# Kernel tuning notes

Hardware: AMD Instinct MI355X
Metric: run time of the kernel (lower is better)

The kernel has to match this reference:

```python
import jax, jax.numpy as jnp
import numpy as np

D, NH, NKV, HD, DFF, W, PLD = 2048, 8, 2, 256, 8192, 512, 256
EPS = 1e-6

def rmsnorm(x, w):
    # Gemma-style RMSNorm with (1 + weight) scaling
    return x * jax.lax.rsqrt(jnp.mean(x * x, axis=-1, keepdims=True) + EPS) * (1.0 + w)

def rmsnorm_nw(x):
    # v_norm: weightless RMSNorm
    return x * jax.lax.rsqrt(jnp.mean(x * x, axis=-1, keepdims=True) + EPS)

def rotate_half(x):
    x1, x2 = jnp.split(x, 2, axis=-1)
    return jnp.concatenate([-x2, x1], axis=-1)

def setup_inputs() -> dict:
    key = jax.random.key(0)
    ks = jax.random.split(key, 24)
    w = lambda k, shp, s=0.02: (jax.random.normal(k, shp, dtype=jnp.float32) * s)
    inp = {
        "hidden_states": jax.random.normal(ks[0], (1, 1, D), dtype=jnp.float32),
        "cos": jax.random.uniform(ks[1], (1, 1, HD), dtype=jnp.float32),
        "sin": jax.random.uniform(ks[2], (1, 1, HD), dtype=jnp.float32),
        "mask": jnp.zeros((1, 1, 1, W), dtype=jnp.float32),
        "kv_cache": jnp.zeros((2, NKV, W, HD), dtype=jnp.float32),
        "per_layer": jax.random.normal(ks[3], (1, 1, PLD), dtype=jnp.float32),
        "ln_in_w": w(ks[4], (D,)),
        "Wq": w(ks[5], (NH * HD, D)),
        "q_norm_w": w(ks[6], (HD,)),
        "Wk": w(ks[7], (NKV * HD, D)),
        "Wv": w(ks[8], (NKV * HD, D)),
        "k_norm_w": w(ks[9], (HD,)),
        "Wo": w(ks[10], (D, NH * HD)),
        "post_attn_ln_w": w(ks[11], (D,)),
        "pre_ffn_ln_w": w(ks[12], (D,)),
        "Wgate": w(ks[13], (DFF, D)),
        "Wup": w(ks[14], (DFF, D)),
        "Wdown": w(ks[15], (D, DFF)),
        "post_ffn_ln_w": w(ks[16], (D,)),
        "Wpl_gate": w(ks[17], (PLD, D)),
        "Wpl_proj": w(ks[18], (D, PLD)),
        "post_pl_ln_w": w(ks[19], (D,)),
        "layer_scalar": jnp.ones((1,), dtype=jnp.float32),
        "ring_pos": 37,
    }
    return inp

def reference(hidden_states, cos, sin, mask, kv_cache, per_layer,
              ln_in_w, Wq, q_norm_w, Wk, Wv, k_norm_w, Wo,
              post_attn_ln_w, pre_ffn_ln_w, Wgate, Wup, Wdown, post_ffn_ln_w,
              Wpl_gate, Wpl_proj, post_pl_ln_w, layer_scalar, ring_pos):
    n_rep = NH // NKV
    x = hidden_states[0, 0]                      # (D,)
    residual = x
    h = rmsnorm(x, ln_in_w)                      # input_layernorm
    c, s = cos[0, 0], sin[0, 0]                  # (HD,)
    # q/k/v projections (seq=1 decode -> GEMV)
    q = (h @ Wq.T).reshape(NH, HD)
    q = rmsnorm(q, q_norm_w)
    q = q * c + rotate_half(q) * s               # RoPE
    k = (h @ Wk.T).reshape(NKV, HD)
    k = rmsnorm(k, k_norm_w)
    k = k * c + rotate_half(k) * s
    v = rmsnorm_nw((h @ Wv.T).reshape(NKV, HD))
    # slice-write into the ring-buffer KV cache
    kv = kv_cache.at[0, :, ring_pos, :].set(k).at[1, :, ring_pos, :].set(v)
    K, V = kv[0], kv[1]                          # (NKV, W, HD)
    # GQA: repeat kv heads n_rep times
    Kx = jnp.repeat(K, n_rep, axis=0)            # (NH, W, HD)
    Vx = jnp.repeat(V, n_rep, axis=0)
    scores = jnp.einsum('hd,hwd->hw', q, Kx) + mask[0, 0, 0]   # no 1/sqrt(hd), as in source
    attn = jax.nn.softmax(scores, axis=-1)
    o = jnp.einsum('hw,hwd->hd', attn, Vx).reshape(NH * HD)
    attn_out = rmsnorm(o @ Wo.T, post_attn_ln_w)
    x = residual + attn_out
    # gated-GELU MLP
    residual = x
    hn = rmsnorm(x, pre_ffn_ln_w)
    gate = jax.nn.gelu(hn @ Wgate.T, approximate=True)
    mlp = ((gate * (hn @ Wup.T)) @ Wdown.T)
    x = residual + rmsnorm(mlp, post_ffn_ln_w)
    # per-layer input gate/projection
    residual = x
    g = jax.nn.gelu(x @ Wpl_gate.T, approximate=True) * per_layer[0, 0]
    g = rmsnorm(g @ Wpl_proj.T, post_pl_ln_w)
    x = (residual + g) * layer_scalar[0]
    return x.reshape(1, 1, D)

if __name__ == '__main__':
    out = reference(**setup_inputs())
    print(out.shape, out.dtype)
```

## Files before the change

### kernel.cpp

```cpp
#include <hip/hip_runtime.h>
#include <math.h>

#define D 2048
#define NH 8
#define NKV 2
#define HD 256
#define DFF 8192
#define W 512
#define PLD 256
#define EPS 1e-6f

typedef float f32x4 __attribute__((ext_vector_type(4)));

__device__ __forceinline__ f32x4 ntld(const float* p) {
    return __builtin_nontemporal_load(reinterpret_cast<const f32x4*>(p));
}
__device__ __forceinline__ f32x4 ld4(const float* p) {
    return *reinterpret_cast<const f32x4*>(p);
}
__device__ __forceinline__ float dot4(f32x4 a, f32x4 b, float acc) {
    return fmaf(a.x, b.x, fmaf(a.y, b.y, fmaf(a.z, b.z, fmaf(a.w, b.w, acc))));
}

__device__ __forceinline__ float warp_sum(float v) {
    #pragma unroll
    for (int off = 32; off > 0; off >>= 1) v += __shfl_down(v, off, 64);
    return v;
}
__device__ __forceinline__ float warp_max(float v) {
    #pragma unroll
    for (int off = 32; off > 0; off >>= 1) v = fmaxf(v, __shfl_down(v, off, 64));
    return v;
}

__device__ __forceinline__ float block_sum256(float v, float* s4) {
    int lane = threadIdx.x & 63, wid = threadIdx.x >> 6;
    v = warp_sum(v);
    if (lane == 0) s4[wid] = v;
    __syncthreads();
    float r = s4[0] + s4[1] + s4[2] + s4[3];
    __syncthreads();
    return r;
}
__device__ __forceinline__ float block_max256(float v, float* s4) {
    int lane = threadIdx.x & 63, wid = threadIdx.x >> 6;
    v = warp_max(v);
    if (lane == 0) s4[wid] = v;
    __syncthreads();
    float r = fmaxf(fmaxf(s4[0], s4[1]), fmaxf(s4[2], s4[3]));
    __syncthreads();
    return r;
}

__device__ __forceinline__ float gelu_tanh(float x) {
    const float c = 0.7978845608028654f;
    float t = tanhf(c * (x + 0.044715f * x * x * x));
    return 0.5f * x * (1.0f + t);
}

__global__ void rms_in_kernel(const float* __restrict__ x, const float* __restrict__ w,
                              float* __restrict__ out) {
    __shared__ float s4[4];
    int t = threadIdx.x;
    float v[8], ss = 0.f;
    #pragma unroll
    for (int i = 0; i < 8; i++) { v[i] = x[t + i * 256]; ss += v[i] * v[i]; }
    float tot = block_sum256(ss, s4);
    float rs = rsqrtf(tot / (float)D + EPS);
    #pragma unroll
    for (int i = 0; i < 8; i++) out[t + i * 256] = v[i] * rs * (1.f + w[t + i * 256]);
}

__global__ void gemv_qkv_nt(const float* __restrict__ Wq, const float* __restrict__ Wk,
                            const float* __restrict__ Wv, const float* __restrict__ h,
                            float* __restrict__ qraw, float* __restrict__ kraw,
                            float* __restrict__ vraw) {
    int lane = threadIdx.x & 63, wid = threadIdx.x >> 6;
    int row = blockIdx.x * 4 + wid;
    const float* wr;
    float* out;
    if (row < 2048)      { wr = Wq + (size_t)row * D;          out = qraw + row; }
    else if (row < 2560) { wr = Wk + (size_t)(row - 2048) * D; out = kraw + (row - 2048); }
    else                 { wr = Wv + (size_t)(row - 2560) * D; out = vraw + (row - 2560); }
    f32x4 w[8], xv[8];
    #pragma unroll
    for (int c = 0; c < 8; c++) w[c] = ntld(wr + c * 256 + lane * 4);
    #pragma unroll
    for (int c = 0; c < 8; c++) xv[c] = ld4(h + c * 256 + lane * 4);
    float acc = 0.f;
    #pragma unroll
    for (int c = 0; c < 8; c++) acc = dot4(w[c], xv[c], acc);
    acc = warp_sum(acc);
    if (lane == 0) *out = acc;
}

template <int MODE>
__global__ void gemv2048_nt(const float* __restrict__ Wm, const float* __restrict__ x,
                            const float* __restrict__ aux, float* __restrict__ y) {
    int lane = threadIdx.x & 63, wid = threadIdx.x >> 6;
    int row = blockIdx.x * 4 + wid;
    const float* wr = Wm + (size_t)row * D;
    f32x4 w[8], xv[8];
    #pragma unroll
    for (int c = 0; c < 8; c++) w[c] = ntld(wr + c * 256 + lane * 4);
    #pragma unroll
    for (int c = 0; c < 8; c++) xv[c] = ld4(x + c * 256 + lane * 4);
    float acc = 0.f;
    #pragma unroll
    for (int c = 0; c < 8; c++) acc = dot4(w[c], xv[c], acc);
    acc = warp_sum(acc);
    if (lane == 0) {
        if (MODE == 0) y[row] = acc;
        else           y[row] = gelu_tanh(acc) * aux[row];
    }
}

__global__ void gateup_nt(const float* __restrict__ Wg, const float* __restrict__ Wu,
                          const float* __restrict__ hn, float* __restrict__ act) {
    int lane = threadIdx.x & 63, wid = threadIdx.x >> 6;
    int row = blockIdx.x * 4 + wid;
    const float* wg = Wg + (size_t)row * D;
    const float* wu = Wu + (size_t)row * D;
    f32x4 g[8], u[8], xv[8];
    #pragma unroll
    for (int c = 0; c < 8; c++) g[c] = ntld(wg + c * 256 + lane * 4);
    #pragma unroll
    for (int c = 0; c < 8; c++) u[c] = ntld(wu + c * 256 + lane * 4);
    #pragma unroll
    for (int c = 0; c < 8; c++) xv[c] = ld4(hn + c * 256 + lane * 4);
    float ag = 0.f, au = 0.f;
    #pragma unroll
    for (int c = 0; c < 8; c++) { ag = dot4(g[c], xv[c], ag); au = dot4(u[c], xv[c], au); }
    ag = warp_sum(ag);
    au = warp_sum(au);
    if (lane == 0) act[row] = gelu_tanh(ag) * au;
}

__global__ void down_nt(const float* __restrict__ Wd, const float* __restrict__ act,
                        float* __restrict__ y) {
    int lane = threadIdx.x & 63, wid = threadIdx.x >> 6;
    int row = blockIdx.x * 4 + wid;
    const float* wr = Wd + (size_t)row * DFF;
    f32x4 wA[8], wB[8], a[8];
    float acc = 0.f;
    #pragma unroll
    for (int c = 0; c < 8; c++) wA[c] = ntld(wr + c * 256 + lane * 4);
    #pragma unroll
    for (int c = 0; c < 8; c++) wB[c] = ntld(wr + 2048 + c * 256 + lane * 4);
    #pragma unroll
    for (int c = 0; c < 8; c++) a[c] = ld4(act + c * 256 + lane * 4);
    #pragma unroll
    for (int c = 0; c < 8; c++) acc = dot4(wA[c], a[c], acc);
    #pragma unroll
    for (int c = 0; c < 8; c++) wA[c] = ntld(wr + 4096 + c * 256 + lane * 4);
    #pragma unroll
    for (int c = 0; c < 8; c++) a[c] = ld4(act + 2048 + c * 256 + lane * 4);
    #pragma unroll
    for (int c = 0; c < 8; c++) acc = dot4(wB[c], a[c], acc);
    #pragma unroll
    for (int c = 0; c < 8; c++) wB[c] = ntld(wr + 6144 + c * 256 + lane * 4);
    #pragma unroll
    for (int c = 0; c < 8; c++) a[c] = ld4(act + 4096 + c * 256 + lane * 4);
    #pragma unroll
    for (int c = 0; c < 8; c++) acc = dot4(wA[c], a[c], acc);
    #pragma unroll
    for (int c = 0; c < 8; c++) a[c] = ld4(act + 6144 + c * 256 + lane * 4);
    #pragma unroll
    for (int c = 0; c < 8; c++) acc = dot4(wB[c], a[c], acc);
    acc = warp_sum(acc);
    if (lane == 0) y[row] = acc;
}

__global__ void gemv256_nt(const float* __restrict__ Wm, const float* __restrict__ x,
                           float* __restrict__ y) {
    int lane = threadIdx.x & 63, wid = threadIdx.x >> 6;
    int row = blockIdx.x * 4 + wid;
    const float* wr = Wm + (size_t)row * PLD;
    f32x4 w0 = ntld(wr + lane * 4);
    f32x4 x0 = ld4(x + lane * 4);
    float acc = dot4(w0, x0, 0.f);
    acc = warp_sum(acc);
    if (lane == 0) y[row] = acc;
}

__global__ void head_norm_rope(const float* __restrict__ qraw, const float* __restrict__ kraw,
                               const float* __restrict__ vraw, const float* __restrict__ qw,
                               const float* __restrict__ kw, const float* __restrict__ cosv,
                               const float* __restrict__ sinv, float* __restrict__ qf,
                               float* __restrict__ kf, float* __restrict__ vf) {
    __shared__ float s4[4];
    __shared__ float sn[HD];
    int b = blockIdx.x, t = threadIdx.x;
    const float* in; float* out; const float* w; bool rope;
    if (b < 8)       { in = qraw + b * HD;        out = qf + b * HD;        w = qw;      rope = true;  }
    else if (b < 10) { in = kraw + (b - 8) * HD;  out = kf + (b - 8) * HD;  w = kw;      rope = true;  }
    else             { in = vraw + (b - 10) * HD; out = vf + (b - 10) * HD; w = nullptr; rope = false; }
    float x = in[t];
    float tot = block_sum256(x * x, s4);
    float rs = rsqrtf(tot / (float)HD + EPS);
    float nv = x * rs * (w ? (1.f + w[t]) : 1.f);
    sn[t] = nv;
    __syncthreads();
    float o = nv;
    if (rope) {
        float rh = (t < HD / 2) ? -sn[t + HD / 2] : sn[t - HD / 2];
        o = nv * cosv[t] + rh * sinv[t];
    }
    out[t] = o;
}

__global__ void attn_scores(const float* __restrict__ kvc, const float* __restrict__ kf,
                            const float* __restrict__ mask, const float* __restrict__ qf,
                            const int* __restrict__ ring_p, float* __restrict__ scores) {
    int head = blockIdx.x >> 3, wc = blockIdx.x & 7;
    int kvh = head >> 2;
    int lane = threadIdx.x & 63, wid = threadIdx.x >> 6;
    int ring = *ring_p;
    f32x4 qv = ld4(qf + head * HD + lane * 4);
    const float* Kbase = kvc + (size_t)kvh * W * HD;
    #pragma unroll 4
    for (int i = 0; i < 16; i++) {
        int w = wc * 64 + wid * 16 + i;
        const float* krow = (w == ring) ? (kf + kvh * HD) : (Kbase + (size_t)w * HD);
        f32x4 kv4 = ld4(krow + lane * 4);
        float acc = dot4(qv, kv4, 0.f);
        acc = warp_sum(acc);
        if (lane == 0) scores[head * W + w] = acc + mask[w];
    }
}

__global__ void attn_softmax(float* __restrict__ scores, float* __restrict__ attn_o) {
    __shared__ float s4[4];
    int head = blockIdx.x, t = threadIdx.x;
    float s0 = scores[head * W + t], s1 = scores[head * W + 256 + t];
    float m = block_max256(fmaxf(s0, s1), s4);
    float e0 = expf(s0 - m), e1 = expf(s1 - m);
    float sum = block_sum256(e0 + e1, s4);
    float inv = 1.f / sum;
    scores[head * W + t] = e0 * inv;
    scores[head * W + 256 + t] = e1 * inv;
    attn_o[head * HD + t] = 0.f;
}

__global__ void attn_o_partial(const float* __restrict__ kvc, const float* __restrict__ vf,
                               const float* __restrict__ p, const int* __restrict__ ring_p,
                               float* __restrict__ attn_o) {
    int head = blockIdx.x >> 3, wc = blockIdx.x & 7;
    int kvh = head >> 2;
    int d = threadIdx.x;
    int ring = *ring_p;
    const float* Vbase = kvc + (size_t)(NKV + kvh) * W * HD;
    float acc = 0.f;
    #pragma unroll 4
    for (int i = 0; i < 64; i++) {
        int w = wc * 64 + i;
        float pw = p[head * W + w];
        const float* vrow = (w == ring) ? (vf + kvh * HD) : (Vbase + (size_t)w * HD);
        acc = fmaf(pw, vrow[d], acc);
    }
    atomicAdd(&attn_o[head * HD + d], acc);
}

__global__ void post_attn_fused(const float* __restrict__ res, const float* __restrict__ y,
                                const float* __restrict__ w1, const float* __restrict__ w2,
                                float* __restrict__ x1, float* __restrict__ hn) {
    __shared__ float s4[4];
    int t = threadIdx.x;
    float yv[8], ss = 0.f;
    #pragma unroll
    for (int i = 0; i < 8; i++) { yv[i] = y[t + i * 256]; ss += yv[i] * yv[i]; }
    float tot = block_sum256(ss, s4);
    float rs = rsqrtf(tot / (float)D + EPS);
    float xv[8]; ss = 0.f;
    #pragma unroll
    for (int i = 0; i < 8; i++) {
        int idx = t + i * 256;
        float v = res[idx] + yv[i] * rs * (1.f + w1[idx]);
        xv[i] = v; x1[idx] = v; ss += v * v;
    }
    tot = block_sum256(ss, s4);
    rs = rsqrtf(tot / (float)D + EPS);
    #pragma unroll
    for (int i = 0; i < 8; i++) {
        int idx = t + i * 256;
        hn[idx] = xv[i] * rs * (1.f + w2[idx]);
    }
}

__global__ void residual_rms(const float* __restrict__ res, const float* __restrict__ y,
                             const float* __restrict__ w, float* __restrict__ out) {
    __shared__ float s4[4];
    int t = threadIdx.x;
    float yv[8], ss = 0.f;
    #pragma unroll
    for (int i = 0; i < 8; i++) { yv[i] = y[t + i * 256]; ss += yv[i] * yv[i]; }
    float tot = block_sum256(ss, s4);
    float rs = rsqrtf(tot / (float)D + EPS);
    #pragma unroll
    for (int i = 0; i < 8; i++) {
        int idx = t + i * 256;
        out[idx] = res[idx] + yv[i] * rs * (1.f + w[idx]);
    }
}

__global__ void final_kernel(const float* __restrict__ x2, const float* __restrict__ g2,
                             const float* __restrict__ w, const float* __restrict__ scal,
                             float* __restrict__ out) {
    __shared__ float s4[4];
    int t = threadIdx.x;
    float gv[8], ss = 0.f;
    #pragma unroll
    for (int i = 0; i < 8; i++) { gv[i] = g2[t + i * 256]; ss += gv[i] * gv[i]; }
    float tot = block_sum256(ss, s4);
    float rs = rsqrtf(tot / (float)D + EPS);
    float sc = scal[0];
    #pragma unroll
    for (int i = 0; i < 8; i++) {
        int idx = t + i * 256;
        out[idx] = (x2[idx] + gv[i] * rs * (1.f + w[idx])) * sc;
    }
}

extern "C" void kernel_launch(void* const* d_in, const int* in_sizes, int n_in,
                              void* d_out, int out_size, void* d_ws, size_t ws_size,
                              hipStream_t stream) {
    const float* x_in        = (const float*)d_in[0];
    const float* cosv        = (const float*)d_in[1];
    const float* sinv        = (const float*)d_in[2];
    const float* mask        = (const float*)d_in[3];
    const float* kvc         = (const float*)d_in[4];
    const float* per_layer   = (const float*)d_in[5];
    const float* ln_in_w     = (const float*)d_in[6];
    const float* Wq          = (const float*)d_in[7];
    const float* q_norm_w    = (const float*)d_in[8];
    const float* Wk          = (const float*)d_in[9];
    const float* Wv          = (const float*)d_in[10];
    const float* k_norm_w    = (const float*)d_in[11];
    const float* Wo          = (const float*)d_in[12];
    const float* post_attn_w = (const float*)d_in[13];
    const float* pre_ffn_w   = (const float*)d_in[14];
    const float* Wgate       = (const float*)d_in[15];
    const float* Wup         = (const float*)d_in[16];
    const float* Wdown       = (const float*)d_in[17];
    const float* post_ffn_w  = (const float*)d_in[18];
    const float* Wpl_gate    = (const float*)d_in[19];
    const float* Wpl_proj    = (const float*)d_in[20];
    const float* post_pl_w   = (const float*)d_in[21];
    const float* layer_scal  = (const float*)d_in[22];
    const int*   ring_pos    = (const int*)d_in[23];
    float* out = (float*)d_out;
    float* ws  = (float*)d_ws;

    float* h      = ws;
    float* qraw   = ws + 2048;
    float* kraw   = ws + 4096;
    float* vraw   = ws + 4608;
    float* qf     = ws + 5120;
    float* kf     = ws + 7168;
    float* vf     = ws + 7680;
    float* scores = ws + 8192;
    float* attn_o = ws + 12288;
    float* y_wo   = ws + 14336;
    float* x1     = ws + 16384;
    float* hn     = ws + 18432;
    float* act    = ws + 20480;
    float* y2     = ws + 28672;
    float* x2     = ws + 30720;
    float* g      = ws + 32768;
    float* g2     = ws + 33024;

    rms_in_kernel<<<1, 256, 0, stream>>>(x_in, ln_in_w, h);
    gemv_qkv_nt<<<768, 256, 0, stream>>>(Wq, Wk, Wv, h, qraw, kraw, vraw);
    head_norm_rope<<<12, 256, 0, stream>>>(qraw, kraw, vraw, q_norm_w, k_norm_w,
                                           cosv, sinv, qf, kf, vf);
    attn_scores<<<64, 256, 0, stream>>>(kvc, kf, mask, qf, ring_pos, scores);
    attn_softmax<<<8, 256, 0, stream>>>(scores, attn_o);
    attn_o_partial<<<64, 256, 0, stream>>>(kvc, vf, scores, ring_pos, attn_o);
    gemv2048_nt<0><<<512, 256, 0, stream>>>(Wo, attn_o, nullptr, y_wo);
    post_attn_fused<<<1, 256, 0, stream>>>(x_in, y_wo, post_attn_w, pre_ffn_w, x1, hn);
    gateup_nt<<<2048, 256, 0, stream>>>(Wgate, Wup, hn, act);
    down_nt<<<512, 256, 0, stream>>>(Wdown, act, y2);
    residual_rms<<<1, 256, 0, stream>>>(x1, y2, post_ffn_w, x2);
    gemv2048_nt<1><<<64, 256, 0, stream>>>(Wpl_gate, x2, per_layer, g);
    gemv256_nt<<<512, 256, 0, stream>>>(Wpl_proj, g, g2);
    final_kernel<<<1, 256, 0, stream>>>(x2, g2, post_pl_w, layer_scal, out);
}
```

Baseline: 77.47 us.

## Fuse RMSNorms into GEMV prologues and merge attention into one kernel

Removes the single-block RMSNorm kernels by having every wave recompute the norm redundantly inside the following GEMV (QKV, gate/up, per-layer gate) and the final output. The head norm, RoPE, scores, softmax and PV steps are merged into one 1024-thread kernel per head, which drops the atomics and several launches. This cuts the kernel count from 14 to 8, so there are fewer launch gaps and serial tiny kernels. The cost is redundant norm arithmetic and extra vector loads in every wave, plus the attention now running on only 8 blocks.

```diff
diff --git a/kernel.cpp b/kernel.cpp
--- a/kernel.cpp
+++ b/kernel.cpp
@@ -22,34 +22,15 @@
     return fmaf(a.x, b.x, fmaf(a.y, b.y, fmaf(a.z, b.z, fmaf(a.w, b.w, acc))));
 }
 
-__device__ __forceinline__ float warp_sum(float v) {
-    #pragma unroll
-    for (int off = 32; off > 0; off >>= 1) v += __shfl_down(v, off, 64);
+__device__ __forceinline__ float wave_sum(float v) {
+    #pragma unroll
+    for (int off = 32; off > 0; off >>= 1) v += __shfl_xor(v, off, 64);
     return v;
 }
-__device__ __forceinline__ float warp_max(float v) {
-    #pragma unroll
-    for (int off = 32; off > 0; off >>= 1) v = fmaxf(v, __shfl_down(v, off, 64));
+__device__ __forceinline__ float wave_max(float v) {
+    #pragma unroll
+    for (int off = 32; off > 0; off >>= 1) v = fmaxf(v, __shfl_xor(v, off, 64));
     return v;
-}
-
-__device__ __forceinline__ float block_sum256(float v, float* s4) {
-    int lane = threadIdx.x & 63, wid = threadIdx.x >> 6;
-    v = warp_sum(v);
-    if (lane == 0) s4[wid] = v;
-    __syncthreads();
-    float r = s4[0] + s4[1] + s4[2] + s4[3];
-    __syncthreads();
-    return r;
-}
-__device__ __forceinline__ float block_max256(float v, float* s4) {
-    int lane = threadIdx.x & 63, wid = threadIdx.x >> 6;
-    v = warp_max(v);
-    if (lane == 0) s4[wid] = v;
-    __syncthreads();
-    float r = fmaxf(fmaxf(s4[0], s4[1]), fmaxf(s4[2], s4[3]));
-    __syncthreads();
-    return r;
 }
 
 __device__ __forceinline__ float gelu_tanh(float x) {
@@ -58,267 +39,315 @@
     return 0.5f * x * (1.0f + t);
 }
 
-__global__ void rms_in_kernel(const float* __restrict__ x, const float* __restrict__ w,
-                              float* __restrict__ out) {
-    __shared__ float s4[4];
-    int t = threadIdx.x;
-    float v[8], ss = 0.f;
-    #pragma unroll
-    for (int i = 0; i < 8; i++) { v[i] = x[t + i * 256]; ss += v[i] * v[i]; }
-    float tot = block_sum256(ss, s4);
-    float rs = rsqrtf(tot / (float)D + EPS);
-    #pragma unroll
-    for (int i = 0; i < 8; i++) out[t + i * 256] = v[i] * rs * (1.f + w[t + i * 256]);
-}
-
-__global__ void gemv_qkv_nt(const float* __restrict__ Wq, const float* __restrict__ Wk,
-                            const float* __restrict__ Wv, const float* __restrict__ h,
-                            float* __restrict__ qraw, float* __restrict__ kraw,
-                            float* __restrict__ vraw) {
+__global__ __launch_bounds__(256, 1)
+void qkv_fused(const float* __restrict__ Wq, const float* __restrict__ Wk,
+               const float* __restrict__ Wv, const float* __restrict__ x,
+               const float* __restrict__ lnw, float* __restrict__ qraw,
+               float* __restrict__ kraw, float* __restrict__ vraw) {
     int lane = threadIdx.x & 63, wid = threadIdx.x >> 6;
     int row = blockIdx.x * 4 + wid;
     const float* wr;
-    float* out;
-    if (row < 2048)      { wr = Wq + (size_t)row * D;          out = qraw + row; }
-    else if (row < 2560) { wr = Wk + (size_t)(row - 2048) * D; out = kraw + (row - 2048); }
-    else                 { wr = Wv + (size_t)(row - 2560) * D; out = vraw + (row - 2560); }
-    f32x4 w[8], xv[8];
+    float* outp;
+    if (row < 2048)      { wr = Wq + (size_t)row * D;          outp = qraw + row; }
+    else if (row < 2560) { wr = Wk + (size_t)(row - 2048) * D; outp = kraw + (row - 2048); }
+    else                 { wr = Wv + (size_t)(row - 2560) * D; outp = vraw + (row - 2560); }
+    f32x4 xv[8], lw[8];
+    #pragma unroll
+    for (int c = 0; c < 8; c++) xv[c] = ld4(x + c * 256 + lane * 4);
+    #pragma unroll
+    for (int c = 0; c < 8; c++) lw[c] = ld4(lnw + c * 256 + lane * 4);
+    f32x4 wv4[8];
+    #pragma unroll
+    for (int c = 0; c < 8; c++) wv4[c] = ntld(wr + c * 256 + lane * 4);
+    float ss = 0.f;
+    #pragma unroll
+    for (int c = 0; c < 8; c++) ss = dot4(xv[c], xv[c], ss);
+    ss = wave_sum(ss);
+    float rs = rsqrtf(ss / (float)D + EPS);
+    float acc = 0.f;
+    #pragma unroll
+    for (int c = 0; c < 8; c++) {
+        f32x4 h4 = xv[c] * rs * (1.f + lw[c]);
+        acc = dot4(wv4[c], h4, acc);
+    }
+    acc = wave_sum(acc);
+    if (lane == 0) *outp = acc;
+}
+
+__global__ __launch_bounds__(1024, 1)
+void attn_fused(const float* __restrict__ kvc, const float* __restrict__ qraw,
+                const float* __restrict__ kraw, const float* __restrict__ vraw,
+                const float* __restrict__ qw, const float* __restrict__ kw,
+                const float* __restrict__ cosv, const float* __restrict__ sinv,
+                const float* __restrict__ mask, const int* __restrict__ ring_p,
+                float* __restrict__ attn_o) {
+    __shared__ float qn[HD], kn[HD], vn[HD], p[W], red[16], oacc[4][HD];
+    int t = threadIdx.x, wv = t >> 6, lane = t & 63;
+    int head = blockIdx.x, kvh = head >> 2;
+    int ring = *ring_p;
+    if (wv == 0) {
+        f32x4 v4 = ld4(qraw + head * HD + lane * 4);
+        float ss = wave_sum(dot4(v4, v4, 0.f));
+        float rs = rsqrtf(ss / (float)HD + EPS);
+        f32x4 w4 = ld4(qw + lane * 4);
+        f32x4 nv = v4 * rs * (1.f + w4);
+        f32x4 pr;
+        pr.x = __shfl_xor(nv.x, 32, 64);
+        pr.y = __shfl_xor(nv.y, 32, 64);
+        pr.z = __shfl_xor(nv.z, 32, 64);
+        pr.w = __shfl_xor(nv.w, 32, 64);
+        f32x4 c4 = ld4(cosv + lane * 4), s4 = ld4(sinv + lane * 4);
+        float sgn = (lane < 32) ? -1.f : 1.f;
+        f32x4 o4 = nv * c4 + pr * s4 * sgn;
+        *reinterpret_cast<f32x4*>(qn + lane * 4) = o4;
+    } else if (wv == 1) {
+        f32x4 v4 = ld4(kraw + kvh * HD + lane * 4);
+        float ss = wave_sum(dot4(v4, v4, 0.f));
+        float rs = rsqrtf(ss / (float)HD + EPS);
+        f32x4 w4 = ld4(kw + lane * 4);
+        f32x4 nv = v4 * rs * (1.f + w4);
+        f32x4 pr;
+        pr.x = __shfl_xor(nv.x, 32, 64);
+        pr.y = __shfl_xor(nv.y, 32, 64);
+        pr.z = __shfl_xor(nv.z, 32, 64);
+        pr.w = __shfl_xor(nv.w, 32, 64);
+        f32x4 c4 = ld4(cosv + lane * 4), s4 = ld4(sinv + lane * 4);
+        float sgn = (lane < 32) ? -1.f : 1.f;
+        f32x4 o4 = nv * c4 + pr * s4 * sgn;
+        *reinterpret_cast<f32x4*>(kn + lane * 4) = o4;
+    } else if (wv == 2) {
+        f32x4 v4 = ld4(vraw + kvh * HD + lane * 4);
+        float ss = wave_sum(dot4(v4, v4, 0.f));
+        float rs = rsqrtf(ss / (float)HD + EPS);
+        *reinterpret_cast<f32x4*>(vn + lane * 4) = v4 * rs;
+    }
+    __syncthreads();
+    {
+        f32x4 qq = *reinterpret_cast<f32x4*>(qn + lane * 4);
+        f32x4 krg = *reinterpret_cast<f32x4*>(kn + lane * 4);
+        const float* Kb = kvc + (size_t)kvh * W * HD;
+        #pragma unroll 4
+        for (int i = 0; i < 32; i++) {
+            int w = wv * 32 + i;
+            f32x4 k4 = (w == ring) ? krg : ld4(Kb + (size_t)w * HD + lane * 4);
+            float s = wave_sum(dot4(qq, k4, 0.f));
+            if (lane == 0) p[w] = s + mask[w];
+        }
+    }
+    __syncthreads();
+    float e = 0.f, sv = 0.f;
+    if (t < W) {
+        sv = p[t];
+        float m = wave_max(sv);
+        if (lane == 0) red[wv] = m;
+    }
+    __syncthreads();
+    float m = red[0];
+    #pragma unroll
+    for (int i = 1; i < 8; i++) m = fmaxf(m, red[i]);
+    if (t < W) e = expf(sv - m);
+    __syncthreads();
+    if (t < W) {
+        float se = wave_sum(e);
+        if (lane == 0) red[wv] = se;
+    }
+    __syncthreads();
+    float tot = 0.f;
+    #pragma unroll
+    for (int i = 0; i < 8; i++) tot += red[i];
+    if (t < W) p[t] = e / tot;
+    __syncthreads();
+    {
+        int d = t & 255, q = t >> 8;
+        float vr = vn[d];
+        const float* Vb = kvc + (size_t)(NKV + kvh) * W * HD;
+        float acc = 0.f;
+        #pragma unroll 8
+        for (int i = 0; i < 128; i++) {
+            int w = q * 128 + i;
+            float vv = (w == ring) ? vr : Vb[(size_t)w * HD + d];
+            acc = fmaf(p[w], vv, acc);
+        }
+        oacc[q][d] = acc;
+    }
+    __syncthreads();
+    if (t < HD) attn_o[head * HD + t] = oacc[0][t] + oacc[1][t] + oacc[2][t] + oacc[3][t];
+}
+
+__global__ __launch_bounds__(256, 1)
+void gemv2048_nt(const float* __restrict__ Wm, const float* __restrict__ x,
+                 float* __restrict__ y) {
+    int lane = threadIdx.x & 63, wid = threadIdx.x >> 6;
+    int row = blockIdx.x * 4 + wid;
+    const float* wr = Wm + (size_t)row * D;
+    f32x4 xv[8], w[8];
+    #pragma unroll
+    for (int c = 0; c < 8; c++) xv[c] = ld4(x + c * 256 + lane * 4);
     #pragma unroll
     for (int c = 0; c < 8; c++) w[c] = ntld(wr + c * 256 + lane * 4);
-    #pragma unroll
-    for (int c = 0; c < 8; c++) xv[c] = ld4(h + c * 256 + lane * 4);
     float acc = 0.f;
     #pragma unroll
     for (int c = 0; c < 8; c++) acc = dot4(w[c], xv[c], acc);
-    acc = warp_sum(acc);
-    if (lane == 0) *out = acc;
-}
-
-template <int MODE>
-__global__ void gemv2048_nt(const float* __restrict__ Wm, const float* __restrict__ x,
-                            const float* __restrict__ aux, float* __restrict__ y) {
-    int lane = threadIdx.x & 63, wid = threadIdx.x >> 6;
-    int row = blockIdx.x * 4 + wid;
-    const float* wr = Wm + (size_t)row * D;
-    f32x4 w[8], xv[8];
-    #pragma unroll
-    for (int c = 0; c < 8; c++) w[c] = ntld(wr + c * 256 + lane * 4);
-    #pragma unroll
-    for (int c = 0; c < 8; c++) xv[c] = ld4(x + c * 256 + lane * 4);
-    float acc = 0.f;
-    #pragma unroll
-    for (int c = 0; c < 8; c++) acc = dot4(w[c], xv[c], acc);
-    acc = warp_sum(acc);
-    if (lane == 0) {
-        if (MODE == 0) y[row] = acc;
-        else           y[row] = gelu_tanh(acc) * aux[row];
-    }
-}
-
-__global__ void gateup_nt(const float* __restrict__ Wg, const float* __restrict__ Wu,
-                          const float* __restrict__ hn, float* __restrict__ act) {
+    acc = wave_sum(acc);
+    if (lane == 0) y[row] = acc;
+}
+
+__global__ __launch_bounds__(256, 1)
+void gateup_fused(const float* __restrict__ Wg, const float* __restrict__ Wu,
+                  const float* __restrict__ x, const float* __restrict__ ywo,
+                  const float* __restrict__ w_pa, const float* __restrict__ w_pf,
+                  float* __restrict__ act, float* __restrict__ x1out) {
     int lane = threadIdx.x & 63, wid = threadIdx.x >> 6;
     int row = blockIdx.x * 4 + wid;
     const float* wg = Wg + (size_t)row * D;
     const float* wu = Wu + (size_t)row * D;
-    f32x4 g[8], u[8], xv[8];
-    #pragma unroll
-    for (int c = 0; c < 8; c++) g[c] = ntld(wg + c * 256 + lane * 4);
-    #pragma unroll
-    for (int c = 0; c < 8; c++) u[c] = ntld(wu + c * 256 + lane * 4);
-    #pragma unroll
-    for (int c = 0; c < 8; c++) xv[c] = ld4(hn + c * 256 + lane * 4);
+    f32x4 y4[8], xr4[8], w1[8], w2[8];
+    #pragma unroll
+    for (int c = 0; c < 8; c++) y4[c] = ld4(ywo + c * 256 + lane * 4);
+    #pragma unroll
+    for (int c = 0; c < 8; c++) xr4[c] = ld4(x + c * 256 + lane * 4);
+    #pragma unroll
+    for (int c = 0; c < 8; c++) w1[c] = ld4(w_pa + c * 256 + lane * 4);
+    #pragma unroll
+    for (int c = 0; c < 8; c++) w2[c] = ld4(w_pf + c * 256 + lane * 4);
+    f32x4 g4[8], u4[8];
+    #pragma unroll
+    for (int c = 0; c < 8; c++) g4[c] = ntld(wg + c * 256 + lane * 4);
+    #pragma unroll
+    for (int c = 0; c < 8; c++) u4[c] = ntld(wu + c * 256 + lane * 4);
+    float ss = 0.f;
+    #pragma unroll
+    for (int c = 0; c < 8; c++) ss = dot4(y4[c], y4[c], ss);
+    ss = wave_sum(ss);
+    float rs1 = rsqrtf(ss / (float)D + EPS);
+    f32x4 x1v[8];
+    float s2 = 0.f;
+    #pragma unroll
+    for (int c = 0; c < 8; c++) {
+        f32x4 v = xr4[c] + y4[c] * rs1 * (1.f + w1[c]);
+        x1v[c] = v;
+        s2 = dot4(v, v, s2);
+    }
+    s2 = wave_sum(s2);
+    float rs2 = rsqrtf(s2 / (float)D + EPS);
+    if (blockIdx.x == 0 && wid == 0) {
+        #pragma unroll
+        for (int c = 0; c < 8; c++)
+            *reinterpret_cast<f32x4*>(x1out + c * 256 + lane * 4) = x1v[c];
+    }
     float ag = 0.f, au = 0.f;
     #pragma unroll
-    for (int c = 0; c < 8; c++) { ag = dot4(g[c], xv[c], ag); au = dot4(u[c], xv[c], au); }
-    ag = warp_sum(ag);
-    au = warp_sum(au);
+    for (int c = 0; c < 8; c++) {
+        f32x4 h4 = x1v[c] * rs2 * (1.f + w2[c]);
+        ag = dot4(g4[c], h4, ag);
+        au = dot4(u4[c], h4, au);
+    }
+    ag = wave_sum(ag);
+    au = wave_sum(au);
     if (lane == 0) act[row] = gelu_tanh(ag) * au;
 }
 
-__global__ void down_nt(const float* __restrict__ Wd, const float* __restrict__ act,
-                        float* __restrict__ y) {
+__global__ __launch_bounds__(256, 1)
+void down_nt(const float* __restrict__ Wd, const float* __restrict__ act,
+             float* __restrict__ y) {
     int lane = threadIdx.x & 63, wid = threadIdx.x >> 6;
     int row = blockIdx.x * 4 + wid;
     const float* wr = Wd + (size_t)row * DFF;
     f32x4 wA[8], wB[8], a[8];
     float acc = 0.f;
     #pragma unroll
+    for (int c = 0; c < 8; c++) a[c] = ld4(act + c * 256 + lane * 4);
+    #pragma unroll
     for (int c = 0; c < 8; c++) wA[c] = ntld(wr + c * 256 + lane * 4);
     #pragma unroll
     for (int c = 0; c < 8; c++) wB[c] = ntld(wr + 2048 + c * 256 + lane * 4);
     #pragma unroll
-    for (int c = 0; c < 8; c++) a[c] = ld4(act + c * 256 + lane * 4);
-    #pragma unroll
     for (int c = 0; c < 8; c++) acc = dot4(wA[c], a[c], acc);
     #pragma unroll
+    for (int c = 0; c < 8; c++) a[c] = ld4(act + 2048 + c * 256 + lane * 4);
+    #pragma unroll
     for (int c = 0; c < 8; c++) wA[c] = ntld(wr + 4096 + c * 256 + lane * 4);
     #pragma unroll
-    for (int c = 0; c < 8; c++) a[c] = ld4(act + 2048 + c * 256 + lane * 4);
-    #pragma unroll
     for (int c = 0; c < 8; c++) acc = dot4(wB[c], a[c], acc);
     #pragma unroll
+    for (int c = 0; c < 8; c++) a[c] = ld4(act + 4096 + c * 256 + lane * 4);
+    #pragma unroll
     for (int c = 0; c < 8; c++) wB[c] = ntld(wr + 6144 + c * 256 + lane * 4);
     #pragma unroll
-    for (int c = 0; c < 8; c++) a[c] = ld4(act + 4096 + c * 256 + lane * 4);
-    #pragma unroll
     for (int c = 0; c < 8; c++) acc = dot4(wA[c], a[c], acc);
     #pragma unroll
     for (int c = 0; c < 8; c++) a[c] = ld4(act + 6144 + c * 256 + lane * 4);
     #pragma unroll
     for (int c = 0; c < 8; c++) acc = dot4(wB[c], a[c], acc);
-    acc = warp_sum(acc);
+    acc = wave_sum(acc);
     if (lane == 0) y[row] = acc;
 }
 
-__global__ void gemv256_nt(const float* __restrict__ Wm, const float* __restrict__ x,
-                           float* __restrict__ y) {
-    int lane = threadIdx.x & 63, wid = threadIdx.x >> 6;
-    int row = blockIdx.x * 4 + wid;
-    const float* wr = Wm + (size_t)row * PLD;
-    f32x4 w0 = ntld(wr + lane * 4);
+__global__ __launch_bounds__(256, 1)
+void plgate_fused(const float* __restrict__ Wpl, const float* __restrict__ x1,
+                  const float* __restrict__ y2, const float* __restrict__ w_pf,
+                  const float* __restrict__ per_layer, float* __restrict__ g,
+                  float* __restrict__ x2out) {
+    int lane = threadIdx.x & 63, wid = threadIdx.x >> 6;
+    int row = blockIdx.x * 4 + wid;
+    f32x4 y4[8], x4[8], w4[8];
+    #pragma unroll
+    for (int c = 0; c < 8; c++) y4[c] = ld4(y2 + c * 256 + lane * 4);
+    #pragma unroll
+    for (int c = 0; c < 8; c++) x4[c] = ld4(x1 + c * 256 + lane * 4);
+    #pragma unroll
+    for (int c = 0; c < 8; c++) w4[c] = ld4(w_pf + c * 256 + lane * 4);
+    f32x4 wv4[8];
+    const float* wr = Wpl + (size_t)row * D;
+    #pragma unroll
+    for (int c = 0; c < 8; c++) wv4[c] = ntld(wr + c * 256 + lane * 4);
+    float ss = 0.f;
+    #pragma unroll
+    for (int c = 0; c < 8; c++) ss = dot4(y4[c], y4[c], ss);
+    ss = wave_sum(ss);
+    float rs = rsqrtf(ss / (float)D + EPS);
+    f32x4 x2v[8];
+    #pragma unroll
+    for (int c = 0; c < 8; c++) x2v[c] = x4[c] + y4[c] * rs * (1.f + w4[c]);
+    if (blockIdx.x == 0 && wid == 0) {
+        #pragma unroll
+        for (int c = 0; c < 8; c++)
+            *reinterpret_cast<f32x4*>(x2out + c * 256 + lane * 4) = x2v[c];
+    }
+    float acc = 0.f;
+    #pragma unroll
+    for (int c = 0; c < 8; c++) acc = dot4(wv4[c], x2v[c], acc);
+    acc = wave_sum(acc);
+    if (lane == 0) g[row] = gelu_tanh(acc) * per_layer[row];
+}
+
+__global__ __launch_bounds__(256, 1)
+void gemv256_nt(const float* __restrict__ Wm, const float* __restrict__ x,
+                float* __restrict__ y) {
+    int lane = threadIdx.x & 63, wid = threadIdx.x >> 6;
+    int row = blockIdx.x * 4 + wid;
     f32x4 x0 = ld4(x + lane * 4);
+    f32x4 w0 = ntld(Wm + (size_t)row * PLD + lane * 4);
     float acc = dot4(w0, x0, 0.f);
-    acc = warp_sum(acc);
+    acc = wave_sum(acc);
     if (lane == 0) y[row] = acc;
 }
 
-__global__ void head_norm_rope(const float* __restrict__ qraw, const float* __restrict__ kraw,
-                               const float* __restrict__ vraw, const float* __restrict__ qw,
-                               const float* __restrict__ kw, const float* __restrict__ cosv,
-                               const float* __restrict__ sinv, float* __restrict__ qf,
-                               float* __restrict__ kf, float* __restrict__ vf) {
-    __shared__ float s4[4];
-    __shared__ float sn[HD];
-    int b = blockIdx.x, t = threadIdx.x;
-    const float* in; float* out; const float* w; bool rope;
-    if (b < 8)       { in = qraw + b * HD;        out = qf + b * HD;        w = qw;      rope = true;  }
-    else if (b < 10) { in = kraw + (b - 8) * HD;  out = kf + (b - 8) * HD;  w = kw;      rope = true;  }
-    else             { in = vraw + (b - 10) * HD; out = vf + (b - 10) * HD; w = nullptr; rope = false; }
-    float x = in[t];
-    float tot = block_sum256(x * x, s4);
-    float rs = rsqrtf(tot / (float)HD + EPS);
-    float nv = x * rs * (w ? (1.f + w[t]) : 1.f);
-    sn[t] = nv;
-    __syncthreads();
-    float o = nv;
-    if (rope) {
-        float rh = (t < HD / 2) ? -sn[t + HD / 2] : sn[t - HD / 2];
-        o = nv * cosv[t] + rh * sinv[t];
-    }
-    out[t] = o;
-}
-
-__global__ void attn_scores(const float* __restrict__ kvc, const float* __restrict__ kf,
-                            const float* __restrict__ mask, const float* __restrict__ qf,
-                            const int* __restrict__ ring_p, float* __restrict__ scores) {
-    int head = blockIdx.x >> 3, wc = blockIdx.x & 7;
-    int kvh = head >> 2;
-    int lane = threadIdx.x & 63, wid = threadIdx.x >> 6;
-    int ring = *ring_p;
-    f32x4 qv = ld4(qf + head * HD + lane * 4);
-    const float* Kbase = kvc + (size_t)kvh * W * HD;
-    #pragma unroll 4
-    for (int i = 0; i < 16; i++) {
-        int w = wc * 64 + wid * 16 + i;
-        const float* krow = (w == ring) ? (kf + kvh * HD) : (Kbase + (size_t)w * HD);
-        f32x4 kv4 = ld4(krow + lane * 4);
-        float acc = dot4(qv, kv4, 0.f);
-        acc = warp_sum(acc);
-        if (lane == 0) scores[head * W + w] = acc + mask[w];
-    }
-}
-
-__global__ void attn_softmax(float* __restrict__ scores, float* __restrict__ attn_o) {
-    __shared__ float s4[4];
-    int head = blockIdx.x, t = threadIdx.x;
-    float s0 = scores[head * W + t], s1 = scores[head * W + 256 + t];
-    float m = block_max256(fmaxf(s0, s1), s4);
-    float e0 = expf(s0 - m), e1 = expf(s1 - m);
-    float sum = block_sum256(e0 + e1, s4);
-    float inv = 1.f / sum;
-    scores[head * W + t] = e0 * inv;
-    scores[head * W + 256 + t] = e1 * inv;
-    attn_o[head * HD + t] = 0.f;
-}
-
-__global__ void attn_o_partial(const float* __restrict__ kvc, const float* __restrict__ vf,
-                               const float* __restrict__ p, const int* __restrict__ ring_p,
-                               float* __restrict__ attn_o) {
-    int head = blockIdx.x >> 3, wc = blockIdx.x & 7;
-    int kvh = head >> 2;
-    int d = threadIdx.x;
-    int ring = *ring_p;
-    const float* Vbase = kvc + (size_t)(NKV + kvh) * W * HD;
-    float acc = 0.f;
-    #pragma unroll 4
-    for (int i = 0; i < 64; i++) {
-        int w = wc * 64 + i;
-        float pw = p[head * W + w];
-        const float* vrow = (w == ring) ? (vf + kvh * HD) : (Vbase + (size_t)w * HD);
-        acc = fmaf(pw, vrow[d], acc);
-    }
-    atomicAdd(&attn_o[head * HD + d], acc);
-}
-
-__global__ void post_attn_fused(const float* __restrict__ res, const float* __restrict__ y,
-                                const float* __restrict__ w1, const float* __restrict__ w2,
-                                float* __restrict__ x1, float* __restrict__ hn) {
-    __shared__ float s4[4];
-    int t = threadIdx.x;
-    float yv[8], ss = 0.f;
-    #pragma unroll
-    for (int i = 0; i < 8; i++) { yv[i] = y[t + i * 256]; ss += yv[i] * yv[i]; }
-    float tot = block_sum256(ss, s4);
-    float rs = rsqrtf(tot / (float)D + EPS);
-    float xv[8]; ss = 0.f;
-    #pragma unroll
-    for (int i = 0; i < 8; i++) {
-        int idx = t + i * 256;
-        float v = res[idx] + yv[i] * rs * (1.f + w1[idx]);
-        xv[i] = v; x1[idx] = v; ss += v * v;
-    }
-    tot = block_sum256(ss, s4);
-    rs = rsqrtf(tot / (float)D + EPS);
-    #pragma unroll
-    for (int i = 0; i < 8; i++) {
-        int idx = t + i * 256;
-        hn[idx] = xv[i] * rs * (1.f + w2[idx]);
-    }
-}
-
-__global__ void residual_rms(const float* __restrict__ res, const float* __restrict__ y,
-                             const float* __restrict__ w, float* __restrict__ out) {
-    __shared__ float s4[4];
-    int t = threadIdx.x;
-    float yv[8], ss = 0.f;
-    #pragma unroll
-    for (int i = 0; i < 8; i++) { yv[i] = y[t + i * 256]; ss += yv[i] * yv[i]; }
-    float tot = block_sum256(ss, s4);
-    float rs = rsqrtf(tot / (float)D + EPS);
-    #pragma unroll
-    for (int i = 0; i < 8; i++) {
-        int idx = t + i * 256;
-        out[idx] = res[idx] + yv[i] * rs * (1.f + w[idx]);
-    }
-}
-
-__global__ void final_kernel(const float* __restrict__ x2, const float* __restrict__ g2,
-                             const float* __restrict__ w, const float* __restrict__ scal,
-                             float* __restrict__ out) {
-    __shared__ float s4[4];
-    int t = threadIdx.x;
-    float gv[8], ss = 0.f;
-    #pragma unroll
-    for (int i = 0; i < 8; i++) { gv[i] = g2[t + i * 256]; ss += gv[i] * gv[i]; }
-    float tot = block_sum256(ss, s4);
-    float rs = rsqrtf(tot / (float)D + EPS);
-    float sc = scal[0];
-    #pragma unroll
-    for (int i = 0; i < 8; i++) {
-        int idx = t + i * 256;
-        out[idx] = (x2[idx] + gv[i] * rs * (1.f + w[idx])) * sc;
-    }
+__global__ __launch_bounds__(256, 1)
+void final_fused(const float* __restrict__ x2, const float* __restrict__ g2,
+                 const float* __restrict__ w, const float* __restrict__ scal,
+                 float* __restrict__ out) {
+    int lane = threadIdx.x & 63;
+    f32x4 g4[8];
+    #pragma unroll
+    for (int c = 0; c < 8; c++) g4[c] = ld4(g2 + c * 256 + lane * 4);
+    float ss = 0.f;
+    #pragma unroll
+    for (int c = 0; c < 8; c++) ss = dot4(g4[c], g4[c], ss);
+    ss = wave_sum(ss);
+    float rs = rsqrtf(ss / (float)D + EPS);
+    int idx = blockIdx.x * 256 + threadIdx.x;
+    out[idx] = (x2[idx] + g2[idx] * rs * (1.f + w[idx])) * scal[0];
 }
 
 extern "C" void kernel_launch(void* const* d_in, const int* in_sizes, int n_in,
@@ -351,37 +380,27 @@
     float* out = (float*)d_out;
     float* ws  = (float*)d_ws;
 
-    float* h      = ws;
-    float* qraw   = ws + 2048;
-    float* kraw   = ws + 4096;
-    float* vraw   = ws + 4608;
-    float* qf     = ws + 5120;
-    float* kf     = ws + 7168;
-    float* vf     = ws + 7680;
-    float* scores = ws + 8192;
-    float* attn_o = ws + 12288;
-    float* y_wo   = ws + 14336;
-    float* x1     = ws + 16384;
-    float* hn     = ws + 18432;
-    float* act    = ws + 20480;
-    float* y2     = ws + 28672;
-    float* x2     = ws + 30720;
-    float* g      = ws + 32768;
-    float* g2     = ws + 33024;
-
-    rms_in_kernel<<<1, 256, 0, stream>>>(x_in, ln_in_w, h);
-    gemv_qkv_nt<<<768, 256, 0, stream>>>(Wq, Wk, Wv, h, qraw, kraw, vraw);
-    head_norm_rope<<<12, 256, 0, stream>>>(qraw, kraw, vraw, q_norm_w, k_norm_w,
-                                           cosv, sinv, qf, kf, vf);
-    attn_scores<<<64, 256, 0, stream>>>(kvc, kf, mask, qf, ring_pos, scores);
-    attn_softmax<<<8, 256, 0, stream>>>(scores, attn_o);
-    attn_o_partial<<<64, 256, 0, stream>>>(kvc, vf, scores, ring_pos, attn_o);
-    gemv2048_nt<0><<<512, 256, 0, stream>>>(Wo, attn_o, nullptr, y_wo);
-    post_attn_fused<<<1, 256, 0, stream>>>(x_in, y_wo, post_attn_w, pre_ffn_w, x1, hn);
-    gateup_nt<<<2048, 256, 0, stream>>>(Wgate, Wup, hn, act);
+    float* qraw   = ws;
+    float* kraw   = ws + 2048;
+    float* vraw   = ws + 2560;
+    float* attn_o = ws + 3072;
+    float* y_wo   = ws + 5120;
+    float* x1     = ws + 7168;
+    float* act    = ws + 9216;
+    float* y2     = ws + 17408;
+    float* x2     = ws + 19456;
+    float* g      = ws + 21504;
+    float* g2     = ws + 21760;
+
+    qkv_fused<<<768, 256, 0, stream>>>(Wq, Wk, Wv, x_in, ln_in_w, qraw, kraw, vraw);
+    attn_fused<<<8, 1024, 0, stream>>>(kvc, qraw, kraw, vraw, q_norm_w, k_norm_w,
+                                       cosv, sinv, mask, ring_pos, attn_o);
+    gemv2048_nt<<<512, 256, 0, stream>>>(Wo, attn_o, y_wo);
+    gateup_fused<<<2048, 256, 0, stream>>>(Wgate, Wup, x_in, y_wo,
+                                           post_attn_w, pre_ffn_w, act, x1);
     down_nt<<<512, 256, 0, stream>>>(Wdown, act, y2);
-    residual_rms<<<1, 256, 0, stream>>>(x1, y2, post_ffn_w, x2);
-    gemv2048_nt<1><<<64, 256, 0, stream>>>(Wpl_gate, x2, per_layer, g);
+    plgate_fused<<<64, 256, 0, stream>>>(Wpl_gate, x1, y2, post_ffn_w,
+                                         per_layer, g, x2);
     gemv256_nt<<<512, 256, 0, stream>>>(Wpl_proj, g, g2);
-    final_kernel<<<1, 256, 0, stream>>>(x2, g2, post_pl_w, layer_scal, out);
-}
+    final_fused<<<8, 256, 0, stream>>>(x2, g2, post_pl_w, layer_scal, out);
+}
```

Result: slower. 82.17 us (+6.1%).
